# Optimization experiments

Hardware: AMD Instinct MI355X
Metric: run time of the kernel (lower is better)

## Reference

```python
import jax, jax.numpy as jnp
import numpy as np

B, N, D = 2, 4096, 640      # batch, latent tokens, model dim
H, DH = 8, 80               # heads, head dim (H*DH == D)
CN, CD = 77, 768            # context tokens, context dim (CLIP)
FF = 4 * D                  # GEGLU inner dim = 2560
EPS = 1e-5


def _ln(x, w, b):
    m = jnp.mean(x, axis=-1, keepdims=True)
    v = jnp.mean(jnp.square(x - m), axis=-1, keepdims=True)
    return (x - m) * jax.lax.rsqrt(v + EPS) * w + b


def _attn(xq, xkv, wq, wk, wv, wo, bo):
    b, n, _ = xq.shape
    m = xkv.shape[1]
    q = (xq @ wq).reshape(b, n, H, DH).transpose(0, 2, 1, 3)   # b h n d
    k = (xkv @ wk).reshape(b, m, H, DH).transpose(0, 2, 1, 3)  # b h m d
    v = (xkv @ wv).reshape(b, m, H, DH).transpose(0, 2, 1, 3)
    scores = jnp.einsum('bhid,bhjd->bhij', q, k) * (DH ** -0.5)
    attn = jax.nn.softmax(scores, axis=-1)
    out = jnp.einsum('bhij,bhjd->bhid', attn, v)
    out = out.transpose(0, 2, 1, 3).reshape(b, n, H * DH)
    return out @ wo + bo


def setup_inputs() -> dict:
    key = jax.random.key(0)
    ks = jax.random.split(key, 20)
    s = 0.02
    r = lambda k, sh: (jax.random.normal(k, sh, jnp.float32) * s)
    return {
        'x': jax.random.normal(ks[0], (B, N, D), jnp.float32),
        'context': jax.random.normal(ks[1], (B, CN, CD), jnp.float32),
        'ln1_w': jnp.ones((D,), jnp.float32), 'ln1_b': jnp.zeros((D,), jnp.float32),
        'ln2_w': jnp.ones((D,), jnp.float32), 'ln2_b': jnp.zeros((D,), jnp.float32),
        'ln3_w': jnp.ones((D,), jnp.float32), 'ln3_b': jnp.zeros((D,), jnp.float32),
        'wq1': r(ks[2], (D, D)), 'wk1': r(ks[3], (D, D)), 'wv1': r(ks[4], (D, D)),
        'wo1': r(ks[5], (D, D)), 'bo1': jnp.zeros((D,), jnp.float32),
        'wq2': r(ks[6], (D, D)), 'wk2': r(ks[7], (CD, D)), 'wv2': r(ks[8], (CD, D)),
        'wo2': r(ks[9], (D, D)), 'bo2': jnp.zeros((D,), jnp.float32),
        'w_ff1': r(ks[10], (D, 2 * FF)), 'b_ff1': jnp.zeros((2 * FF,), jnp.float32),
        'w_ff2': r(ks[11], (FF, D)), 'b_ff2': jnp.zeros((D,), jnp.float32),
    }


def reference(x, context,
              ln1_w, ln1_b, ln2_w, ln2_b, ln3_w, ln3_b,
              wq1, wk1, wv1, wo1, bo1,
              wq2, wk2, wv2, wo2, bo2,
              w_ff1, b_ff1, w_ff2, b_ff2):
    # self-attention block
    h = _ln(x, ln1_w, ln1_b)
    x = _attn(h, h, wq1, wk1, wv1, wo1, bo1) + x
    # cross-attention block (k/v from context)
    h = _ln(x, ln2_w, ln2_b)
    x = _attn(h, context, wq2, wk2, wv2, wo2, bo2) + x
    # GEGLU feed-forward
    h = _ln(x, ln3_w, ln3_b)
    proj = h @ w_ff1 + b_ff1
    a, g = jnp.split(proj, 2, axis=-1)
    ff = (a * jax.nn.gelu(g, approximate=False)) @ w_ff2 + b_ff2
    return ff + x
```

## Files before the change

### kernel.cpp

```cpp
#include <hip/hip_runtime.h>
#include <hip/hip_bf16.h>

typedef __hip_bfloat16 bf16;
typedef short s16x8 __attribute__((ext_vector_type(8)));
typedef short s16x4 __attribute__((ext_vector_type(4)));
typedef float f32x4 __attribute__((ext_vector_type(4)));

#define SCALE_DH 0.11180339887498949f
#define QSCALE   0.16129820878f

static __device__ __forceinline__ float b2f(short u) {
  union { float f; unsigned int i; } x;
  x.i = ((unsigned int)(unsigned short)u) << 16;
  return x.f;
}

static __device__ __forceinline__ float tof(float x) { return x; }
static __device__ __forceinline__ float tof(bf16 x) { return __bfloat162float(x); }

static __device__ __forceinline__ void gload16(const bf16* g, bf16* l) {
  __builtin_amdgcn_global_load_lds((__attribute__((address_space(1))) const void*)g,
                                   (__attribute__((address_space(3))) void*)l, 16, 0, 0);
}

struct PrepArgs {
  const float* src[10];
  bf16* dst[10];
  int R[10], C[10], cb[10], base[10];
  int cvtbase;
  const float* ctx;
  bf16* ctxb;
};

__global__ __launch_bounds__(256) void prep_kernel(PrepArgs a) {
  const int bid = blockIdx.x;
  if (bid >= a.cvtbase) {
    const int n = 154 * 768;
    int i = ((bid - a.cvtbase) * 256 + threadIdx.x) * 4;
    if (i + 4 <= n) {
      float4 v = *(const float4*)(a.ctx + i);
      a.ctxb[i + 0] = __float2bfloat16(v.x);
      a.ctxb[i + 1] = __float2bfloat16(v.y);
      a.ctxb[i + 2] = __float2bfloat16(v.z);
      a.ctxb[i + 3] = __float2bfloat16(v.w);
    } else {
      for (int k = i; k < n; ++k) a.ctxb[k] = __float2bfloat16(a.ctx[k]);
    }
    return;
  }
  int jid = 0;
#pragma unroll
  for (int k = 1; k < 10; ++k)
    if (bid >= a.base[k]) jid = k;
  const float* in = a.src[jid];
  bf16* out = a.dst[jid];
  const int R = a.R[jid], C = a.C[jid];
  const int lb = bid - a.base[jid];
  const int cblk = lb % a.cb[jid], rblk = lb / a.cb[jid];
  __shared__ float t[32][33];
  const int tx = threadIdx.x & 31, ty = threadIdx.x >> 5;
  const long r0 = (long)rblk * 32, c0 = (long)cblk * 32;
#pragma unroll
  for (int i = 0; i < 4; ++i)
    t[ty + 8 * i][tx] = in[(r0 + ty + 8 * i) * C + c0 + tx];
  __syncthreads();
#pragma unroll
  for (int i = 0; i < 4; ++i)
    out[(c0 + ty + 8 * i) * R + r0 + tx] = __float2bfloat16(t[tx][ty + 8 * i]);
}

template <typename T>
__global__ __launch_bounds__(256) void ln_kernel(const T* __restrict__ x,
                                                 const float* __restrict__ w,
                                                 const float* __restrict__ b,
                                                 bf16* __restrict__ out) {
  const int wv = threadIdx.x >> 6, l = threadIdx.x & 63;
  const long row = (long)blockIdx.x * 4 + wv;
  const T* xr = x + row * 640;
  float v[10];
  float s = 0.f;
#pragma unroll
  for (int j = 0; j < 10; ++j) { v[j] = tof(xr[l + 64 * j]); s += v[j]; }
#pragma unroll
  for (int o = 32; o > 0; o >>= 1) s += __shfl_xor(s, o);
  const float mean = s * (1.f / 640.f);
  float vs = 0.f;
#pragma unroll
  for (int j = 0; j < 10; ++j) { float d = v[j] - mean; vs += d * d; }
#pragma unroll
  for (int o = 32; o > 0; o >>= 1) vs += __shfl_xor(vs, o);
  const float rstd = rsqrtf(vs * (1.f / 640.f) + 1e-5f);
  bf16* orow = out + row * 640;
#pragma unroll
  for (int j = 0; j < 10; ++j) {
    int d = l + 64 * j;
    orow[d] = __float2bfloat16((v[j] - mean) * rstd * w[d] + b[d]);
  }
}

template <int EPI>
__global__ __launch_bounds__(256) void gemm_kernel(const bf16* __restrict__ A,
                                                   const bf16* __restrict__ Bt,
                                                   const float* __restrict__ bias,
                                                   const float* __restrict__ res,
                                                   void* __restrict__ Cout,
                                                   int M, int K, int ldc) {
  __shared__ bf16 Ash[128 * 64];
  __shared__ bf16 Bsh[128 * 64];
  const int tid = threadIdx.x, w = tid >> 6, l = tid & 63;
  const int m0 = blockIdx.x * 128, n0 = blockIdx.y * 128;
  const int mb = (w >> 1) * 64, nb = (w & 1) * 64;
  const int lo = l & 15, lg = l >> 4, lo7 = l & 7;
  const f32x4 fz = {0.f, 0.f, 0.f, 0.f};
  f32x4 acc[4][4];
#pragma unroll
  for (int i = 0; i < 4; ++i)
#pragma unroll
    for (int j = 0; j < 4; ++j) acc[i][j] = fz;

  const int g = tid;
  const int gr = g >> 3;
  const int gcsw = 8 * ((g & 7) ^ (gr & 7));
  const bf16* pa[4];
  const bf16* pb[4];
  bf16* la[4];
  bf16* lb[4];
#pragma unroll
  for (int s = 0; s < 4; ++s) {
    const int rl = gr + 32 * s;
    int ra = m0 + rl; if (ra >= M) ra = M - 1;
    pa[s] = A + (long)ra * K + gcsw;
    pb[s] = Bt + (long)(n0 + rl) * K + gcsw;
    la[s] = Ash + (g + 256 * s) * 8;
    lb[s] = Bsh + (g + 256 * s) * 8;
  }

  for (int k0 = 0; k0 < K; k0 += 64) {
    __syncthreads();
#pragma unroll
    for (int s = 0; s < 4; ++s) {
      gload16(pa[s], la[s]); pa[s] += 64;
      gload16(pb[s], lb[s]); pb[s] += 64;
    }
    __syncthreads();
#pragma unroll
    for (int kk = 0; kk < 2; ++kk) {
      const int sl = ((kk * 4 + lg) ^ lo7) * 8;
      s16x8 a[4], b[4];
#pragma unroll
      for (int i = 0; i < 4; ++i)
        a[i] = *(const s16x8*)(Ash + (mb + i * 16 + lo) * 64 + sl);
#pragma unroll
      for (int j = 0; j < 4; ++j)
        b[j] = *(const s16x8*)(Bsh + (nb + j * 16 + lo) * 64 + sl);
#pragma unroll
      for (int i = 0; i < 4; ++i)
#pragma unroll
        for (int j = 0; j < 4; ++j)
          acc[i][j] = __builtin_amdgcn_mfma_f32_16x16x32_bf16(a[i], b[j], acc[i][j], 0, 0, 0);
    }
  }
  const int rb = m0 + mb + lg * 4;
  const int cb = n0 + nb + lo;
#pragma unroll
  for (int i = 0; i < 4; ++i) {
#pragma unroll
    for (int j = 0; j < 4; ++j) {
      const int col = cb + j * 16;
      if (EPI == 3 && col >= 1280) {
        const int t = col - 1280;
        const int hh = t / 80, dh = t % 80;
        const int row0 = rb + i * 16;
        const int bb = row0 >> 12, n = row0 & 4095;
        s16x4 pk;
#pragma unroll
        for (int r = 0; r < 4; ++r)
          pk[r] = (short)__bfloat16_as_ushort(__float2bfloat16(acc[i][j][r]));
        bf16* vt = (bf16*)res;
        *(s16x4*)(vt + (long)(bb * 8 + hh) * 327680 + (long)dh * 4096 + n) = pk;
        continue;
      }
#pragma unroll
      for (int r = 0; r < 4; ++r) {
        const int row = rb + i * 16 + r;
        if (row < M)
          ((bf16*)Cout)[(long)row * ldc + col] = __float2bfloat16(acc[i][j][r]);
      }
    }
  }
}

template <int EPI>
__global__ __launch_bounds__(256) void gemm64_kernel(const bf16* __restrict__ A,
                                                     const bf16* __restrict__ Bt,
                                                     const float* __restrict__ bias,
                                                     const void* __restrict__ res,
                                                     void* __restrict__ Cout,
                                                     int K, int ldc) {
  __shared__ bf16 Ash[64 * 64];
  __shared__ bf16 Bsh[128 * 64];
  const int tid = threadIdx.x, w = tid >> 6, l = tid & 63;
  const int m0 = blockIdx.x * 64, n0 = blockIdx.y * 128;
  const int mb = (w & 1) * 32, nb = (w >> 1) * 64;
  const int lo = l & 15, lg = l >> 4, lo7 = l & 7;
  const f32x4 fz = {0.f, 0.f, 0.f, 0.f};
  f32x4 acc[2][4];
#pragma unroll
  for (int i = 0; i < 2; ++i)
#pragma unroll
    for (int j = 0; j < 4; ++j) acc[i][j] = fz;

  const int g = tid;
  const int gr = g >> 3;
  const int gcsw = 8 * ((g & 7) ^ (gr & 7));
  const bf16* pa[2];
  const bf16* pb[4];
  bf16* la[2];
  bf16* lb[4];
#pragma unroll
  for (int s = 0; s < 2; ++s) {
    pa[s] = A + (long)(m0 + gr + 32 * s) * K + gcsw;
    la[s] = Ash + (g + 256 * s) * 8;
  }
#pragma unroll
  for (int s = 0; s < 4; ++s) {
    pb[s] = Bt + (long)(n0 + gr + 32 * s) * K + gcsw;
    lb[s] = Bsh + (g + 256 * s) * 8;
  }

  for (int k0 = 0; k0 < K; k0 += 64) {
    __syncthreads();
#pragma unroll
    for (int s = 0; s < 2; ++s) { gload16(pa[s], la[s]); pa[s] += 64; }
#pragma unroll
    for (int s = 0; s < 4; ++s) { gload16(pb[s], lb[s]); pb[s] += 64; }
    __syncthreads();
#pragma unroll
    for (int kk = 0; kk < 2; ++kk) {
      const int sl = ((kk * 4 + lg) ^ lo7) * 8;
      s16x8 a[2], b[4];
#pragma unroll
      for (int i = 0; i < 2; ++i)
        a[i] = *(const s16x8*)(Ash + (mb + i * 16 + lo) * 64 + sl);
#pragma unroll
      for (int j = 0; j < 4; ++j)
        b[j] = *(const s16x8*)(Bsh + (nb + j * 16 + lo) * 64 + sl);
#pragma unroll
      for (int i = 0; i < 2; ++i)
#pragma unroll
        for (int j = 0; j < 4; ++j)
          acc[i][j] = __builtin_amdgcn_mfma_f32_16x16x32_bf16(a[i], b[j], acc[i][j], 0, 0, 0);
    }
  }
  const int rb = m0 + mb + lg * 4;
  const int cb = n0 + nb + lo;
#pragma unroll
  for (int i = 0; i < 2; ++i) {
#pragma unroll
    for (int j = 0; j < 4; ++j) {
      const int col = cb + j * 16;
      float bv = 0.f;
      if (EPI >= 4) bv = bias[col];
#pragma unroll
      for (int r = 0; r < 4; ++r) {
        const int row = rb + i * 16 + r;
        const long idx = (long)row * ldc + col;
        float v = acc[i][j][r] + bv;
        if (EPI == 4) {
          v += ((const float*)res)[idx];
          ((bf16*)Cout)[idx] = __float2bfloat16(v);
        } else if (EPI == 5) {
          v += __bfloat162float(((const bf16*)res)[idx]);
          ((bf16*)Cout)[idx] = __float2bfloat16(v);
        } else if (EPI == 6) {
          v += __bfloat162float(((const bf16*)res)[idx]);
          ((float*)Cout)[idx] = v;
        } else {
          ((bf16*)Cout)[idx] = __float2bfloat16(v);
        }
      }
    }
  }
}

__global__ __launch_bounds__(256, 3) void flash_kernel(const bf16* __restrict__ qkv,
                                                       const bf16* __restrict__ vT,
                                                       bf16* __restrict__ out) {
  __shared__ bf16 Ksh[2][64 * 80];
  __shared__ bf16 Vsh[2][80 * 64];
  const int bid = blockIdx.x;
  const int xcd = bid & 7, wi = bid >> 3;
  const int bh = xcd * 2 + (wi & 1);
  const int qx = wi >> 1;
  const int b = bh >> 3, h = bh & 7;
  const int tid = threadIdx.x, w = tid >> 6, l = tid & 63;
  const int r0 = qx * 128 + w * 32;
  const int lg = l >> 4, lo = l & 15, lo7 = l & 7;
  const int sb = l & 48;
  const s16x8 sz = {0, 0, 0, 0, 0, 0, 0, 0};
  const f32x4 fz = {0.f, 0.f, 0.f, 0.f};

  s16x8 qa[2][3];
#pragma unroll
  for (int gq = 0; gq < 2; ++gq) {
    const bf16* qp = qkv + (long)(b * 4096 + r0 + gq * 16 + lo) * 1920 + h * 80;
    qa[gq][0] = *(const s16x8*)(qp + lg * 8);
    qa[gq][1] = *(const s16x8*)(qp + 32 + lg * 8);
    qa[gq][2] = (lg < 2) ? *(const s16x8*)(qp + 64 + lg * 8) : sz;
#pragma unroll
    for (int f = 0; f < 3; ++f) {
      s16x8 q = qa[gq][f], r;
#pragma unroll
      for (int i = 0; i < 8; ++i)
        r[i] = (short)(__bfloat16_as_ushort(__float2bfloat16(b2f(q[i]) * QSCALE)));
      qa[gq][f] = r;
    }
  }

  const bf16* kp[3];
  const int nbatch = (w < 2) ? 3 : 2;
#pragma unroll
  for (int it = 0; it < 3; ++it) {
    int g = tid + 256 * it;
    int gc = (g < 640) ? g : 0;
    int krow = gc / 10, ksl = gc % 10;
    int ksrc = (ksl < 8) ? (ksl ^ (krow & 7)) : (8 + ((ksl - 8) ^ ((krow >> 2) & 1)));
    kp[it] = qkv + (long)(b * 4096 + krow) * 1920 + 640 + h * 80 + ksrc * 8;
  }
  const bf16* vp0 = vT + (long)bh * 327680 + (long)(tid >> 3) * 4096 +
                    (((tid & 7) ^ ((tid >> 3) & 7)) * 8);
  const int soff0 = tid * 8;

  const int voff0 = (((lg >> 1) + 0) ^ lo7) * 8 + 4 * (lg & 1);
  const int voff1 = (((lg >> 1) + 2) ^ lo7) * 8 + 4 * (lg & 1);
  const int voff2 = (((lg >> 1) + 4) ^ lo7) * 8 + 4 * (lg & 1);
  const int voff3 = (((lg >> 1) + 6) ^ lo7) * 8 + 4 * (lg & 1);

  float lrA = 0.f, lrB = 0.f;
  f32x4 oA[5], oB[5];
#pragma unroll
  for (int dt = 0; dt < 5; ++dt) { oA[dt] = fz; oB[dt] = fz; }

#pragma unroll
  for (int it = 0; it < 3; ++it) {
    if (it < nbatch) {
      gload16(kp[it], Ksh[0] + soff0 + 2048 * it); kp[it] += 64 * 1920;
      gload16(vp0 + (long)it * 131072, Vsh[0] + soff0 + 2048 * it);
    }
  }
  __syncthreads();

  for (int kt = 0; kt < 64; ++kt) {
    const int cur = kt & 1;
    const bf16* kbuf = Ksh[cur];
    const bf16* vbuf = Vsh[cur];

    if (kt < 63) {
#pragma unroll
      for (int it = 0; it < 3; ++it) {
        if (it < nbatch) {
          gload16(kp[it], Ksh[cur ^ 1] + soff0 + 2048 * it); kp[it] += 64 * 1920;
          gload16(vp0 + (long)(kt + 1) * 64 + (long)it * 131072, Vsh[cur ^ 1] + soff0 + 2048 * it);
        }
      }
    }

    unsigned paA[8], paB[8];
    f32x4 s0A, s0B, s1A, s1B;
    {
      s16x8 kb0 = *(const s16x8*)(kbuf + lo * 80 + ((lg ^ lo7)) * 8);
      s16x8 kb1 = *(const s16x8*)(kbuf + lo * 80 + (((4 + lg) ^ lo7)) * 8);
      s16x8 kb2 = (lg < 2) ? *(const s16x8*)(kbuf + lo * 80 + 64 + ((lg ^ ((lo >> 2) & 1))) * 8) : sz;
      __builtin_amdgcn_s_setprio(1);
      s0A = __builtin_amdgcn_mfma_f32_16x16x32_bf16(kb0, qa[0][0], fz, 0, 0, 0);
      s0A = __builtin_amdgcn_mfma_f32_16x16x32_bf16(kb1, qa[0][1], s0A, 0, 0, 0);
      s0A = __builtin_amdgcn_mfma_f32_16x16x32_bf16(kb2, qa[0][2], s0A, 0, 0, 0);
      s0B = __builtin_amdgcn_mfma_f32_16x16x32_bf16(kb0, qa[1][0], fz, 0, 0, 0);
      s0B = __builtin_amdgcn_mfma_f32_16x16x32_bf16(kb1, qa[1][1], s0B, 0, 0, 0);
      s0B = __builtin_amdgcn_mfma_f32_16x16x32_bf16(kb2, qa[1][2], s0B, 0, 0, 0);
      __builtin_amdgcn_s_setprio(0);
    }
#pragma unroll
    for (int ntl = 1; ntl <= 4; ++ntl) {
      if (ntl < 4) {
        s16x8 kb0 = *(const s16x8*)(kbuf + (ntl * 16 + lo) * 80 + ((lg ^ lo7)) * 8);
        s16x8 kb1 = *(const s16x8*)(kbuf + (ntl * 16 + lo) * 80 + (((4 + lg) ^ lo7)) * 8);
        s16x8 kb2 = (lg < 2)
                        ? *(const s16x8*)(kbuf + (ntl * 16 + lo) * 80 + 64 + ((lg ^ ((lo >> 2) & 1))) * 8)
                        : sz;
        __builtin_amdgcn_s_setprio(1);
        s1A = __builtin_amdgcn_mfma_f32_16x16x32_bf16(kb0, qa[0][0], fz, 0, 0, 0);
        s1A = __builtin_amdgcn_mfma_f32_16x16x32_bf16(kb1, qa[0][1], s1A, 0, 0, 0);
        s1A = __builtin_amdgcn_mfma_f32_16x16x32_bf16(kb2, qa[0][2], s1A, 0, 0, 0);
        s1B = __builtin_amdgcn_mfma_f32_16x16x32_bf16(kb0, qa[1][0], fz, 0, 0, 0);
        s1B = __builtin_amdgcn_mfma_f32_16x16x32_bf16(kb1, qa[1][1], s1B, 0, 0, 0);
        s1B = __builtin_amdgcn_mfma_f32_16x16x32_bf16(kb2, qa[1][2], s1B, 0, 0, 0);
        __builtin_amdgcn_s_setprio(0);
      }
      {
        const int pidx = ntl - 1;
        float a0 = __builtin_amdgcn_exp2f(s0A[0]);
        float a1 = __builtin_amdgcn_exp2f(s0A[1]);
        float a2 = __builtin_amdgcn_exp2f(s0A[2]);
        float a3 = __builtin_amdgcn_exp2f(s0A[3]);
        lrA += (a0 + a1) + (a2 + a3);
        unsigned u0, u1;
        asm("v_cvt_pk_bf16_f32 %0, %1, %2" : "=v"(u0) : "v"(a0), "v"(a1));
        asm("v_cvt_pk_bf16_f32 %0, %1, %2" : "=v"(u1) : "v"(a2), "v"(a3));
        paA[pidx * 2] = u0;
        paA[pidx * 2 + 1] = u1;
        float b0 = __builtin_amdgcn_exp2f(s0B[0]);
        float b1 = __builtin_amdgcn_exp2f(s0B[1]);
        float b2 = __builtin_amdgcn_exp2f(s0B[2]);
        float b3 = __builtin_amdgcn_exp2f(s0B[3]);
        lrB += (b0 + b1) + (b2 + b3);
        asm("v_cvt_pk_bf16_f32 %0, %1, %2" : "=v"(u0) : "v"(b0), "v"(b1));
        asm("v_cvt_pk_bf16_f32 %0, %1, %2" : "=v"(u1) : "v"(b2), "v"(b3));
        paB[pidx * 2] = u0;
        paB[pidx * 2 + 1] = u1;
      }
      s0A = s1A;
      s0B = s1B;
    }

    typedef unsigned u32x2 __attribute__((ext_vector_type(2)));
    s16x8 frA0, frA1, frB0, frB1;
    {
      u32x2* p;
      p = (u32x2*)&frA0; p[0] = (u32x2){paA[0], paA[1]}; p[1] = (u32x2){paA[2], paA[3]};
      p = (u32x2*)&frA1; p[0] = (u32x2){paA[4], paA[5]}; p[1] = (u32x2){paA[6], paA[7]};
      p = (u32x2*)&frB0; p[0] = (u32x2){paB[0], paB[1]}; p[1] = (u32x2){paB[2], paB[3]};
      p = (u32x2*)&frB1; p[0] = (u32x2){paB[4], paB[5]}; p[1] = (u32x2){paB[6], paB[7]};
    }

    __builtin_amdgcn_s_setprio(1);
#pragma unroll
    for (int dt = 0; dt < 5; ++dt) {
      const bf16* vrow = vbuf + (dt * 16 + lo) * 64;
      s16x4 w00 = *(const s16x4*)(vrow + voff0);
      s16x4 w01 = *(const s16x4*)(vrow + voff1);
      s16x4 w10 = *(const s16x4*)(vrow + voff2);
      s16x4 w11 = *(const s16x4*)(vrow + voff3);
      s16x8 vb0 = __builtin_shufflevector(w00, w01, 0, 1, 2, 3, 4, 5, 6, 7);
      s16x8 vb1 = __builtin_shufflevector(w10, w11, 0, 1, 2, 3, 4, 5, 6, 7);
      oA[dt] = __builtin_amdgcn_mfma_f32_16x16x32_bf16(frA0, vb0, oA[dt], 0, 0, 0);
      oA[dt] = __builtin_amdgcn_mfma_f32_16x16x32_bf16(frA1, vb1, oA[dt], 0, 0, 0);
      oB[dt] = __builtin_amdgcn_mfma_f32_16x16x32_bf16(frB0, vb0, oB[dt], 0, 0, 0);
      oB[dt] = __builtin_amdgcn_mfma_f32_16x16x32_bf16(frB1, vb1, oB[dt], 0, 0, 0);
    }
    __builtin_amdgcn_s_setprio(0);

    __syncthreads();
  }

  {
    float ssum = lrA;
    ssum += __shfl_xor(ssum, 16);
    ssum += __shfl_xor(ssum, 32);
    const float linv = 1.f / ssum;
    float li[4];
#pragma unroll
    for (int r = 0; r < 4; ++r) li[r] = __shfl(linv, sb + lg * 4 + r);
    bf16* ob = out + (long)(b * 4096 + r0 + lg * 4) * 640 + h * 80 + lo;
#pragma unroll
    for (int r = 0; r < 4; ++r)
#pragma unroll
      for (int dt = 0; dt < 5; ++dt)
        ob[(long)r * 640 + dt * 16] = __float2bfloat16(oA[dt][r] * li[r]);
  }
  {
    float ssum = lrB;
    ssum += __shfl_xor(ssum, 16);
    ssum += __shfl_xor(ssum, 32);
    const float linv = 1.f / ssum;
    float li[4];
#pragma unroll
    for (int r = 0; r < 4; ++r) li[r] = __shfl(linv, sb + lg * 4 + r);
    bf16* ob = out + (long)(b * 4096 + r0 + 16 + lg * 4) * 640 + h * 80 + lo;
#pragma unroll
    for (int r = 0; r < 4; ++r)
#pragma unroll
      for (int dt = 0; dt < 5; ++dt)
        ob[(long)r * 640 + dt * 16] = __float2bfloat16(oB[dt][r] * li[r]);
  }
}

__global__ __launch_bounds__(256) void cross_kernel(const bf16* __restrict__ q2,
                                                    const bf16* __restrict__ kv2,
                                                    bf16* __restrict__ out) {
  __shared__ bf16 Ksh2[80 * 88];
  __shared__ bf16 Vsh2[80 * 88];
  const int bh = blockIdx.y, b = bh >> 3, h = bh & 7;
  const int tid = threadIdx.x, w = tid >> 6, l = tid & 63;
  const int r0 = blockIdx.x * 128 + w * 32;
  const int lg = l >> 4, lo = l & 15;
  const int sb = l & 48;
  const s16x8 sz = {0, 0, 0, 0, 0, 0, 0, 0};
  const f32x4 fz = {0.f, 0.f, 0.f, 0.f};

  s16x8 qa[2][3];
#pragma unroll
  for (int gq = 0; gq < 2; ++gq) {
    const bf16* qp = q2 + (long)(b * 4096 + r0 + gq * 16 + lo) * 640 + h * 80;
    qa[gq][0] = *(const s16x8*)(qp + lg * 8);
    qa[gq][1] = *(const s16x8*)(qp + 32 + lg * 8);
    qa[gq][2] = (lg < 2) ? *(const s16x8*)(qp + 64 + lg * 8) : sz;
#pragma unroll
    for (int f = 0; f < 3; ++f) {
      s16x8 q = qa[gq][f], r;
#pragma unroll
      for (int i = 0; i < 8; ++i)
        r[i] = (short)(__bfloat16_as_ushort(__float2bfloat16(b2f(q[i]) * QSCALE)));
      qa[gq][f] = r;
    }
  }

  for (int c = tid; c < 800; c += 256) {
    int row = c / 10, s = c % 10;
    s16x8 v = sz;
    if (row < 77)
      v = *(const s16x8*)(kv2 + (long)(b * 77 + row) * 1280 + h * 80 + s * 8);
    *(s16x8*)(Ksh2 + row * 88 + s * 8) = v;
  }
  for (int c = tid; c < 770; c += 256) {
    int j = c / 10, d8 = (c % 10) * 8;
    s16x8 v = *(const s16x8*)(kv2 + (long)(b * 77 + j) * 1280 + 640 + h * 80 + d8);
    const short* vs = (const short*)&v;
#pragma unroll
    for (int i = 0; i < 8; ++i) ((short*)Vsh2)[(d8 + i) * 88 + j] = vs[i];
  }
  if (tid < 240) {
    int d = tid / 3, j = 77 + tid % 3;
    ((short*)Vsh2)[d * 88 + j] = 0;
  }
  __syncthreads();

  float lrA = 0.f, lrB = 0.f;
  f32x4 oA[5], oB[5];
#pragma unroll
  for (int dt = 0; dt < 5; ++dt) { oA[dt] = fz; oB[dt] = fz; }

  unsigned paA[10], paB[10];
  f32x4 s0A, s0B, s1A, s1B;
  {
    s16x8 kb0 = *(const s16x8*)(Ksh2 + lo * 88 + lg * 8);
    s16x8 kb1 = *(const s16x8*)(Ksh2 + lo * 88 + 32 + lg * 8);
    s16x8 kb2 = (lg < 2) ? *(const s16x8*)(Ksh2 + lo * 88 + 64 + lg * 8) : sz;
    __builtin_amdgcn_s_setprio(1);
    s0A = __builtin_amdgcn_mfma_f32_16x16x32_bf16(kb0, qa[0][0], fz, 0, 0, 0);
    s0A = __builtin_amdgcn_mfma_f32_16x16x32_bf16(kb1, qa[0][1], s0A, 0, 0, 0);
    s0A = __builtin_amdgcn_mfma_f32_16x16x32_bf16(kb2, qa[0][2], s0A, 0, 0, 0);
    s0B = __builtin_amdgcn_mfma_f32_16x16x32_bf16(kb0, qa[1][0], fz, 0, 0, 0);
    s0B = __builtin_amdgcn_mfma_f32_16x16x32_bf16(kb1, qa[1][1], s0B, 0, 0, 0);
    s0B = __builtin_amdgcn_mfma_f32_16x16x32_bf16(kb2, qa[1][2], s0B, 0, 0, 0);
    __builtin_amdgcn_s_setprio(0);
  }
#pragma unroll
  for (int ntl = 1; ntl <= 5; ++ntl) {
    if (ntl < 5) {
      s16x8 kb0 = *(const s16x8*)(Ksh2 + (ntl * 16 + lo) * 88 + lg * 8);
      s16x8 kb1 = *(const s16x8*)(Ksh2 + (ntl * 16 + lo) * 88 + 32 + lg * 8);
      s16x8 kb2 = (lg < 2) ? *(const s16x8*)(Ksh2 + (ntl * 16 + lo) * 88 + 64 + lg * 8) : sz;
      __builtin_amdgcn_s_setprio(1);
      s1A = __builtin_amdgcn_mfma_f32_16x16x32_bf16(kb0, qa[0][0], fz, 0, 0, 0);
      s1A = __builtin_amdgcn_mfma_f32_16x16x32_bf16(kb1, qa[0][1], s1A, 0, 0, 0);
      s1A = __builtin_amdgcn_mfma_f32_16x16x32_bf16(kb2, qa[0][2], s1A, 0, 0, 0);
      s1B = __builtin_amdgcn_mfma_f32_16x16x32_bf16(kb0, qa[1][0], fz, 0, 0, 0);
      s1B = __builtin_amdgcn_mfma_f32_16x16x32_bf16(kb1, qa[1][1], s1B, 0, 0, 0);
      s1B = __builtin_amdgcn_mfma_f32_16x16x32_bf16(kb2, qa[1][2], s1B, 0, 0, 0);
      __builtin_amdgcn_s_setprio(0);
    }
    {
      const int pidx = ntl - 1;
      float a0 = __builtin_amdgcn_exp2f(s0A[0]);
      float a1 = __builtin_amdgcn_exp2f(s0A[1]);
      float a2 = __builtin_amdgcn_exp2f(s0A[2]);
      float a3 = __builtin_amdgcn_exp2f(s0A[3]);
      float b0 = __builtin_amdgcn_exp2f(s0B[0]);
      float b1 = __builtin_amdgcn_exp2f(s0B[1]);
      float b2 = __builtin_amdgcn_exp2f(s0B[2]);
      float b3 = __builtin_amdgcn_exp2f(s0B[3]);
      if (pidx == 4) {
        if (lg * 4 + 1 >= 13) { a1 = 0.f; b1 = 0.f; }
        if (lg * 4 + 2 >= 13) { a2 = 0.f; b2 = 0.f; }
        if (lg * 4 + 3 >= 13) { a3 = 0.f; b3 = 0.f; }
      }
      lrA += (a0 + a1) + (a2 + a3);
      lrB += (b0 + b1) + (b2 + b3);
      unsigned u0, u1;
      asm("v_cvt_pk_bf16_f32 %0, %1, %2" : "=v"(u0) : "v"(a0), "v"(a1));
      asm("v_cvt_pk_bf16_f32 %0, %1, %2" : "=v"(u1) : "v"(a2), "v"(a3));
      paA[pidx * 2] = u0;
      paA[pidx * 2 + 1] = u1;
      asm("v_cvt_pk_bf16_f32 %0, %1, %2" : "=v"(u0) : "v"(b0), "v"(b1));
      asm("v_cvt_pk_bf16_f32 %0, %1, %2" : "=v"(u1) : "v"(b2), "v"(b3));
      paB[pidx * 2] = u0;
      paB[pidx * 2 + 1] = u1;
    }
    s0A = s1A;
    s0B = s1B;
  }

  typedef unsigned u32x2 __attribute__((ext_vector_type(2)));
  s16x8 frA0, frA1, frA2, frB0, frB1, frB2;
  {
    u32x2* p;
    p = (u32x2*)&frA0; p[0] = (u32x2){paA[0], paA[1]}; p[1] = (u32x2){paA[2], paA[3]};
    p = (u32x2*)&frA1; p[0] = (u32x2){paA[4], paA[5]}; p[1] = (u32x2){paA[6], paA[7]};
    p = (u32x2*)&frA2; p[0] = (u32x2){paA[8], paA[9]}; p[1] = (u32x2){0u, 0u};
    p = (u32x2*)&frB0; p[0] = (u32x2){paB[0], paB[1]}; p[1] = (u32x2){paB[2], paB[3]};
    p = (u32x2*)&frB1; p[0] = (u32x2){paB[4], paB[5]}; p[1] = (u32x2){paB[6], paB[7]};
    p = (u32x2*)&frB2; p[0] = (u32x2){paB[8], paB[9]}; p[1] = (u32x2){0u, 0u};
  }

  __builtin_amdgcn_s_setprio(1);
#pragma unroll
  for (int dt = 0; dt < 5; ++dt) {
    const bf16* vrow = Vsh2 + (dt * 16 + lo) * 88;
    s16x4 w00 = *(const s16x4*)(vrow + 4 * lg);
    s16x4 w01 = *(const s16x4*)(vrow + 16 + 4 * lg);
    s16x4 w10 = *(const s16x4*)(vrow + 32 + 4 * lg);
    s16x4 w11 = *(const s16x4*)(vrow + 48 + 4 * lg);
    s16x4 w20 = *(const s16x4*)(vrow + 64 + 4 * lg);
    s16x8 vb0 = __builtin_shufflevector(w00, w01, 0, 1, 2, 3, 4, 5, 6, 7);
    s16x8 vb1 = __builtin_shufflevector(w10, w11, 0, 1, 2, 3, 4, 5, 6, 7);
    s16x8 vb2 = __builtin_shufflevector(w20, w20, 0, 1, 2, 3, 0, 1, 2, 3);
    oA[dt] = __builtin_amdgcn_mfma_f32_16x16x32_bf16(frA0, vb0, oA[dt], 0, 0, 0);
    oA[dt] = __builtin_amdgcn_mfma_f32_16x16x32_bf16(frA1, vb1, oA[dt], 0, 0, 0);
    oA[dt] = __builtin_amdgcn_mfma_f32_16x16x32_bf16(frA2, vb2, oA[dt], 0, 0, 0);
    oB[dt] = __builtin_amdgcn_mfma_f32_16x16x32_bf16(frB0, vb0, oB[dt], 0, 0, 0);
    oB[dt] = __builtin_amdgcn_mfma_f32_16x16x32_bf16(frB1, vb1, oB[dt], 0, 0, 0);
    oB[dt] = __builtin_amdgcn_mfma_f32_16x16x32_bf16(frB2, vb2, oB[dt], 0, 0, 0);
  }
  __builtin_amdgcn_s_setprio(0);

  {
    float ssum = lrA;
    ssum += __shfl_xor(ssum, 16);
    ssum += __shfl_xor(ssum, 32);
    const float linv = 1.f / ssum;
    float li[4];
#pragma unroll
    for (int r = 0; r < 4; ++r) li[r] = __shfl(linv, sb + lg * 4 + r);
    bf16* ob = out + (long)(b * 4096 + r0 + lg * 4) * 640 + h * 80 + lo;
#pragma unroll
    for (int r = 0; r < 4; ++r)
#pragma unroll
      for (int dt = 0; dt < 5; ++dt)
        ob[(long)r * 640 + dt * 16] = __float2bfloat16(oA[dt][r] * li[r]);
  }
  {
    float ssum = lrB;
    ssum += __shfl_xor(ssum, 16);
    ssum += __shfl_xor(ssum, 32);
    const float linv = 1.f / ssum;
    float li[4];
#pragma unroll
    for (int r = 0; r < 4; ++r) li[r] = __shfl(linv, sb + lg * 4 + r);
    bf16* ob = out + (long)(b * 4096 + r0 + 16 + lg * 4) * 640 + h * 80 + lo;
#pragma unroll
    for (int r = 0; r < 4; ++r)
#pragma unroll
      for (int dt = 0; dt < 5; ++dt)
        ob[(long)r * 640 + dt * 16] = __float2bfloat16(oB[dt][r] * li[r]);
  }
}

__global__ __launch_bounds__(256) void geglu_kernel(const bf16* __restrict__ A,
                                                    const bf16* __restrict__ Bt,
                                                    const float* __restrict__ bias,
                                                    bf16* __restrict__ Cout) {
  __shared__ bf16 Ash[128 * 64];
  __shared__ bf16 Bsh[2][64 * 64];
  const int tid = threadIdx.x, w = tid >> 6, l = tid & 63;
  const int m0 = blockIdx.x * 128, n0 = blockIdx.y * 64;
  const int lo = l & 15, lg = l >> 4, lo7 = l & 7;
  const int mb = w * 32;
  const f32x4 fz = {0.f, 0.f, 0.f, 0.f};
  f32x4 accA[2][4], accG[2][4];
#pragma unroll
  for (int i = 0; i < 2; ++i)
#pragma unroll
    for (int j = 0; j < 4; ++j) { accA[i][j] = fz; accG[i][j] = fz; }

  const int g = tid;
  const int gr = g >> 3;
  const int gcsw = 8 * ((g & 7) ^ (gr & 7));
  const bf16* pa[4];
  const bf16* pb[2][2];
  bf16* la[4];
  bf16* lb[2][2];
#pragma unroll
  for (int s = 0; s < 4; ++s) {
    pa[s] = A + (long)(m0 + gr + 32 * s) * 640 + gcsw;
    la[s] = Ash + (g + 256 * s) * 8;
  }
#pragma unroll
  for (int q = 0; q < 2; ++q)
#pragma unroll
    for (int s = 0; s < 2; ++s) {
      pb[q][s] = Bt + (long)(n0 + q * 2560 + gr + 32 * s) * 640 + gcsw;
      lb[q][s] = Bsh[q] + (g + 256 * s) * 8;
    }

  for (int k0 = 0; k0 < 640; k0 += 64) {
    __syncthreads();
#pragma unroll
    for (int s = 0; s < 4; ++s) { gload16(pa[s], la[s]); pa[s] += 64; }
#pragma unroll
    for (int q = 0; q < 2; ++q)
#pragma unroll
      for (int s = 0; s < 2; ++s) { gload16(pb[q][s], lb[q][s]); pb[q][s] += 64; }
    __syncthreads();
#pragma unroll
    for (int kk = 0; kk < 2; ++kk) {
      const int sl = ((kk * 4 + lg) ^ lo7) * 8;
      s16x8 a[2], ba[4], bg[4];
#pragma unroll
      for (int i = 0; i < 2; ++i)
        a[i] = *(const s16x8*)(Ash + (mb + i * 16 + lo) * 64 + sl);
#pragma unroll
      for (int j = 0; j < 4; ++j) {
        ba[j] = *(const s16x8*)(Bsh[0] + (j * 16 + lo) * 64 + sl);
        bg[j] = *(const s16x8*)(Bsh[1] + (j * 16 + lo) * 64 + sl);
      }
#pragma unroll
      for (int i = 0; i < 2; ++i)
#pragma unroll
        for (int j = 0; j < 4; ++j) {
          accA[i][j] = __builtin_amdgcn_mfma_f32_16x16x32_bf16(a[i], ba[j], accA[i][j], 0, 0, 0);
          accG[i][j] = __builtin_amdgcn_mfma_f32_16x16x32_bf16(a[i], bg[j], accG[i][j], 0, 0, 0);
        }
    }
  }
#pragma unroll
  for (int i = 0; i < 2; ++i) {
#pragma unroll
    for (int j = 0; j < 4; ++j) {
      const int col = n0 + j * 16 + lo;
      const float bA = bias[col];
      const float bG = bias[2560 + col];
#pragma unroll
      for (int r = 0; r < 4; ++r) {
        const long row = m0 + mb + i * 16 + lg * 4 + r;
        const float av = accA[i][j][r] + bA;
        const float gv = accG[i][j][r] + bG;
        const float ge = 0.5f * gv * (1.f + erff(gv * 0.70710678118654752f));
        Cout[row * 2560 + col] = __float2bfloat16(av * ge);
      }
    }
  }
}

extern "C" void kernel_launch(void* const* d_in, const int* in_sizes, int n_in,
                              void* d_out, int out_size, void* d_ws, size_t ws_size,
                              hipStream_t stream) {
  (void)in_sizes; (void)n_in; (void)out_size; (void)ws_size;
  const float* x    = (const float*)d_in[0];
  const float* ctx  = (const float*)d_in[1];
  const float* ln1w = (const float*)d_in[2];
  const float* ln1b = (const float*)d_in[3];
  const float* ln2w = (const float*)d_in[4];
  const float* ln2b = (const float*)d_in[5];
  const float* ln3w = (const float*)d_in[6];
  const float* ln3b = (const float*)d_in[7];
  const float* wq1  = (const float*)d_in[8];
  const float* wk1  = (const float*)d_in[9];
  const float* wv1  = (const float*)d_in[10];
  const float* wo1  = (const float*)d_in[11];
  const float* bo1  = (const float*)d_in[12];
  const float* wq2  = (const float*)d_in[13];
  const float* wk2  = (const float*)d_in[14];
  const float* wv2  = (const float*)d_in[15];
  const float* wo2  = (const float*)d_in[16];
  const float* bo2  = (const float*)d_in[17];
  const float* wff1 = (const float*)d_in[18];
  const float* bff1 = (const float*)d_in[19];
  const float* wff2 = (const float*)d_in[20];
  const float* bff2 = (const float*)d_in[21];

  char* ws = (char*)d_ws;
  bf16* Wqkv1 = (bf16*)(ws + 0);
  bf16* Wo1t  = (bf16*)(ws + 2457600);
  bf16* Wq2t  = (bf16*)(ws + 3276800);
  bf16* Wkv2t = (bf16*)(ws + 4096000);
  bf16* Wo2t  = (bf16*)(ws + 6062080);
  bf16* Wff1t = (bf16*)(ws + 6881280);
  bf16* Wff2t = (bf16*)(ws + 13434880);
  bf16* Ctxb  = (bf16*)(ws + 16711680);
  bf16* Hln   = (bf16*)(ws + 16948224);
  bf16* X2b   = (bf16*)(ws + 27433984);
  bf16* X3b   = (bf16*)(ws + 48405504);
  bf16* Qkv   = (bf16*)(ws + 69377024);
  bf16* Ffin  = Qkv;
  bf16* Vt    = (bf16*)(ws + 100834304);
  bf16* Ao    = (bf16*)(ws + 111320064);
  bf16* Q2    = (bf16*)(ws + 121805824);
  bf16* Kv2   = (bf16*)(ws + 132291584);
  float* Outf = (float*)d_out;

  dim3 blk(256);

  PrepArgs pa;
  const float* srcs[10] = {wq1, wk1, wv1, wo1, wq2, wk2, wv2, wo2, wff1, wff2};
  bf16* dsts[10] = {Wqkv1, Wqkv1 + 640 * 640, Wqkv1 + 2 * 640 * 640, Wo1t, Wq2t,
                    Wkv2t, Wkv2t + 640 * 768, Wo2t, Wff1t, Wff2t};
  int Rs[10] = {640, 640, 640, 640, 640, 768, 768, 640, 640, 2560};
  int Cs[10] = {640, 640, 640, 640, 640, 640, 640, 640, 5120, 640};
  int baseacc = 0;
  for (int j = 0; j < 10; ++j) {
    pa.src[j] = srcs[j];
    pa.dst[j] = dsts[j];
    pa.R[j] = Rs[j];
    pa.C[j] = Cs[j];
    pa.cb[j] = Cs[j] / 32;
    pa.base[j] = baseacc;
    baseacc += (Cs[j] / 32) * (Rs[j] / 32);
  }
  pa.cvtbase = baseacc;
  pa.ctx = ctx;
  pa.ctxb = Ctxb;
  const int prep_blocks = baseacc + 116;
  prep_kernel<<<prep_blocks, blk, 0, stream>>>(pa);

  ln_kernel<float><<<2048, blk, 0, stream>>>(x, ln1w, ln1b, Hln);
  gemm_kernel<3><<<dim3(64, 15), blk, 0, stream>>>(Hln, Wqkv1, nullptr, (const float*)Vt, Qkv, 8192, 640, 1920);
  flash_kernel<<<512, blk, 0, stream>>>(Qkv, Vt, Ao);
  gemm64_kernel<4><<<dim3(128, 5), blk, 0, stream>>>(Ao, Wo1t, bo1, x, X2b, 640, 640);
  ln_kernel<bf16><<<2048, blk, 0, stream>>>(X2b, ln2w, ln2b, Hln);
  gemm64_kernel<0><<<dim3(128, 5), blk, 0, stream>>>(Hln, Wq2t, nullptr, nullptr, Q2, 640, 640);
  gemm_kernel<0><<<dim3(2, 10), blk, 0, stream>>>(Ctxb, Wkv2t, nullptr, nullptr, Kv2, 154, 768, 1280);
  cross_kernel<<<dim3(32, 16), blk, 0, stream>>>(Q2, Kv2, Ao);
  gemm64_kernel<5><<<dim3(128, 5), blk, 0, stream>>>(Ao, Wo2t, bo2, X2b, X3b, 640, 640);
  ln_kernel<bf16><<<2048, blk, 0, stream>>>(X3b, ln3w, ln3b, Hln);
  geglu_kernel<<<dim3(64, 40), blk, 0, stream>>>(Hln, Wff1t, bff1, Ffin);
  gemm64_kernel<6><<<dim3(128, 5), blk, 0, stream>>>(Ffin, Wff2t, bff2, X3b, Outf, 2560, 640);
}
```

Measured before the change: 341.1 us.

## Split self-attention KV range in two and add a combine kernel

The flash kernel now processes half of the key/value sequence per block. This doubles the grid to 1024 blocks so more of the GPU's block slots are filled. Each half writes an unnormalized bf16 partial output and its softmax row sums. A new comb_kernel adds the two partials and divides by the combined sum. This relies on the kernel not using a running max, and it adds an extra launch, the partial-buffer traffic and one more bf16 rounding of intermediate values.

```diff
diff --git a/kernel.cpp b/kernel.cpp
--- a/kernel.cpp
+++ b/kernel.cpp
@@ -285,18 +285,21 @@
 
 __global__ __launch_bounds__(256, 3) void flash_kernel(const bf16* __restrict__ qkv,
                                                        const bf16* __restrict__ vT,
-                                                       bf16* __restrict__ out) {
+                                                       bf16* __restrict__ OP0,
+                                                       bf16* __restrict__ OP1,
+                                                       float* __restrict__ L) {
   __shared__ bf16 Ksh[2][64 * 80];
   __shared__ bf16 Vsh[2][80 * 64];
   const int bid = blockIdx.x;
   const int xcd = bid & 7, wi = bid >> 3;
   const int bh = xcd * 2 + (wi & 1);
-  const int qx = wi >> 1;
+  const int rest = wi >> 1;
+  const int qx = rest & 31;
+  const int z = rest >> 5;
   const int b = bh >> 3, h = bh & 7;
   const int tid = threadIdx.x, w = tid >> 6, l = tid & 63;
   const int r0 = qx * 128 + w * 32;
   const int lg = l >> 4, lo = l & 15, lo7 = l & 7;
-  const int sb = l & 48;
   const s16x8 sz = {0, 0, 0, 0, 0, 0, 0, 0};
   const f32x4 fz = {0.f, 0.f, 0.f, 0.f};
 
@@ -325,9 +328,9 @@
     int gc = (g < 640) ? g : 0;
     int krow = gc / 10, ksl = gc % 10;
     int ksrc = (ksl < 8) ? (ksl ^ (krow & 7)) : (8 + ((ksl - 8) ^ ((krow >> 2) & 1)));
-    kp[it] = qkv + (long)(b * 4096 + krow) * 1920 + 640 + h * 80 + ksrc * 8;
-  }
-  const bf16* vp0 = vT + (long)bh * 327680 + (long)(tid >> 3) * 4096 +
+    kp[it] = qkv + (long)(b * 4096 + z * 2048 + krow) * 1920 + 640 + h * 80 + ksrc * 8;
+  }
+  const bf16* vp0 = vT + (long)bh * 327680 + (long)(tid >> 3) * 4096 + z * 2048 +
                     (((tid & 7) ^ ((tid >> 3) & 7)) * 8);
   const int soff0 = tid * 8;
 
@@ -350,12 +353,12 @@
   }
   __syncthreads();
 
-  for (int kt = 0; kt < 64; ++kt) {
+  for (int kt = 0; kt < 32; ++kt) {
     const int cur = kt & 1;
     const bf16* kbuf = Ksh[cur];
     const bf16* vbuf = Vsh[cur];
 
-    if (kt < 63) {
+    if (kt < 31) {
 #pragma unroll
       for (int it = 0; it < 3; ++it) {
         if (it < nbatch) {
@@ -453,35 +456,62 @@
     __syncthreads();
   }
 
+  bf16* OPz = (z == 0) ? OP0 : OP1;
+  float* Lz = L + (long)z * 65536 + (long)bh * 4096;
   {
     float ssum = lrA;
     ssum += __shfl_xor(ssum, 16);
     ssum += __shfl_xor(ssum, 32);
-    const float linv = 1.f / ssum;
-    float li[4];
-#pragma unroll
-    for (int r = 0; r < 4; ++r) li[r] = __shfl(linv, sb + lg * 4 + r);
-    bf16* ob = out + (long)(b * 4096 + r0 + lg * 4) * 640 + h * 80 + lo;
+    if (l < 16) Lz[r0 + l] = ssum;
+    bf16* ob = OPz + (long)(b * 4096 + r0 + lg * 4) * 640 + h * 80 + lo;
 #pragma unroll
     for (int r = 0; r < 4; ++r)
 #pragma unroll
       for (int dt = 0; dt < 5; ++dt)
-        ob[(long)r * 640 + dt * 16] = __float2bfloat16(oA[dt][r] * li[r]);
+        ob[(long)r * 640 + dt * 16] = __float2bfloat16(oA[dt][r]);
   }
   {
     float ssum = lrB;
     ssum += __shfl_xor(ssum, 16);
     ssum += __shfl_xor(ssum, 32);
-    const float linv = 1.f / ssum;
-    float li[4];
-#pragma unroll
-    for (int r = 0; r < 4; ++r) li[r] = __shfl(linv, sb + lg * 4 + r);
-    bf16* ob = out + (long)(b * 4096 + r0 + 16 + lg * 4) * 640 + h * 80 + lo;
+    if (l < 16) Lz[r0 + 16 + l] = ssum;
+    bf16* ob = OPz + (long)(b * 4096 + r0 + 16 + lg * 4) * 640 + h * 80 + lo;
 #pragma unroll
     for (int r = 0; r < 4; ++r)
 #pragma unroll
       for (int dt = 0; dt < 5; ++dt)
-        ob[(long)r * 640 + dt * 16] = __float2bfloat16(oB[dt][r] * li[r]);
+        ob[(long)r * 640 + dt * 16] = __float2bfloat16(oB[dt][r]);
+  }
+}
+
+__global__ __launch_bounds__(256) void comb_kernel(const bf16* __restrict__ OP0,
+                                                   const bf16* __restrict__ OP1,
+                                                   const float* __restrict__ L,
+                                                   bf16* __restrict__ out) {
+  const int wv = threadIdx.x >> 6, l = threadIdx.x & 63;
+  const int row = blockIdx.x * 4 + wv;
+  const int b = row >> 12, n = row & 4095;
+  float linv = 0.f;
+  if (l < 8) {
+    const long li = (long)(b * 8 + l) * 4096 + n;
+    linv = 1.f / (L[li] + L[65536 + li]);
+  }
+  const bf16* p0 = OP0 + (long)row * 640;
+  const bf16* p1 = OP1 + (long)row * 640;
+  bf16* o = out + (long)row * 640;
+#pragma unroll
+  for (int t = 0; t < 2; ++t) {
+    const int g = (t == 0) ? l : 64 + l;
+    if (t == 0 || l < 16) {
+      const float inv = __shfl(linv, g / 10);
+      s16x8 v0 = *(const s16x8*)(p0 + g * 8);
+      s16x8 v1 = *(const s16x8*)(p1 + g * 8);
+      s16x8 r;
+#pragma unroll
+      for (int i = 0; i < 8; ++i)
+        r[i] = (short)__bfloat16_as_ushort(__float2bfloat16((b2f(v0[i]) + b2f(v1[i])) * inv));
+      *(s16x8*)(o + g * 8) = r;
+    }
   }
 }
 
@@ -797,6 +827,9 @@
   bf16* Ao    = (bf16*)(ws + 111320064);
   bf16* Q2    = (bf16*)(ws + 121805824);
   bf16* Kv2   = (bf16*)(ws + 132291584);
+  bf16* OP0   = (bf16*)(ws + 27433984);
+  bf16* OP1   = (bf16*)(ws + 48405504);
+  float* Lpar = (float*)(ws + 59000000);
   float* Outf = (float*)d_out;
 
   dim3 blk(256);
@@ -825,7 +858,8 @@
 
   ln_kernel<float><<<2048, blk, 0, stream>>>(x, ln1w, ln1b, Hln);
   gemm_kernel<3><<<dim3(64, 15), blk, 0, stream>>>(Hln, Wqkv1, nullptr, (const float*)Vt, Qkv, 8192, 640, 1920);
-  flash_kernel<<<512, blk, 0, stream>>>(Qkv, Vt, Ao);
+  flash_kernel<<<1024, blk, 0, stream>>>(Qkv, Vt, OP0, OP1, Lpar);
+  comb_kernel<<<2048, blk, 0, stream>>>(OP0, OP1, Lpar, Ao);
   gemm64_kernel<4><<<dim3(128, 5), blk, 0, stream>>>(Ao, Wo1t, bo1, x, X2b, 640, 640);
   ln_kernel<bf16><<<2048, blk, 0, stream>>>(X2b, ln2w, ln2b, Hln);
   gemm64_kernel<0><<<dim3(128, 5), blk, 0, stream>>>(Hln, Wq2t, nullptr, nullptr, Q2, 640, 640);
```

New measurement: 356.0 us. 4.4% more time.
